# Performance work log

Hardware: AMD Instinct MI355X
Metric: run time of the kernel (lower is better)

Reference implementation:

```python
import jax, jax.numpy as jnp
import numpy as np

NUM_EXPERTS = 8
TOP_K = 2
D_MODEL = 1024
D_HID = 4096
BATCH, SEQ = 2, 2048


def setup_inputs() -> dict:
    key = jax.random.key(0)
    ks = jax.random.split(key, 5)
    s = 0.02  # param scale
    return {
        "x": jax.random.normal(ks[0], (BATCH, SEQ, D_MODEL), dtype=jnp.float32),
        "Wg": jax.random.normal(ks[1], (D_MODEL, NUM_EXPERTS), dtype=jnp.float32) * s,
        "bg": jnp.zeros((NUM_EXPERTS,), dtype=jnp.float32),
        "W0": jax.random.normal(ks[2], (NUM_EXPERTS, D_MODEL, D_HID), dtype=jnp.float32) * s,
        "b0": jnp.zeros((NUM_EXPERTS, D_HID), dtype=jnp.float32),
        "W1": jax.random.normal(ks[3], (NUM_EXPERTS, D_MODEL, D_HID), dtype=jnp.float32) * s,
        "b1": jnp.zeros((NUM_EXPERTS, D_HID), dtype=jnp.float32),
        "W2": jax.random.normal(ks[4], (NUM_EXPERTS, D_HID, D_MODEL), dtype=jnp.float32) * s,
        "b2": jnp.zeros((NUM_EXPERTS, D_MODEL), dtype=jnp.float32),
    }


def reference(x, Wg, bg, W0, b0, W1, b1, W2, b2):
    n, s, d = x.shape
    # --- routing ---
    gate_logits = x @ Wg + bg                      # [n, s, E]
    top_vals, top_idx = jax.lax.top_k(gate_logits, TOP_K)  # [n, s, K]
    w = jax.nn.softmax(top_vals, axis=-1)          # [n, s, K]
    # combine weights scattered back to dense [n, s, E]
    combine = jnp.sum(jax.nn.one_hot(top_idx, NUM_EXPERTS, dtype=x.dtype) * w[..., None], axis=-2)
    # --- dense expert compute (all experts on all tokens, masked combine) ---
    xf = x.reshape(n * s, d)                       # [T, d]
    h = jnp.einsum('td,edh->eth', xf, W0) + b0[:, None, :]   # [E, T, H]
    g = jax.nn.silu(jnp.einsum('td,edh->eth', xf, W1) + b1[:, None, :])
    y = jnp.einsum('eth,ehd->etd', h * g, W2) + b2[:, None, :]  # [E, T, d]
    out = jnp.einsum('te,etd->td', combine.reshape(n * s, NUM_EXPERTS), y)
    return out.reshape(n, s, d)
```

## Files before the change

kernel.cpp:

```cpp
#include <hip/hip_runtime.h>

#define NTOK 4096
#define DM 1024
#define DH 4096
#define NE 8

typedef __attribute__((ext_vector_type(8))) short bf16x8;
typedef __attribute__((ext_vector_type(4))) float f32x4;

__device__ __forceinline__ ushort f2bf(float f) {
  union { float f; unsigned u; } v; v.f = f;
  unsigned r = v.u + 0x7fffu + ((v.u >> 16) & 1u);
  return (ushort)(r >> 16);
}

#define GL2LDS(g, l) __builtin_amdgcn_global_load_lds( \
    (__attribute__((address_space(1))) const void*)(g), \
    (__attribute__((address_space(3))) void*)(l), 16, 0, 0)

__global__ __launch_bounds__(256) void gate_kernel(
    const float* __restrict__ x, const float* __restrict__ Wg,
    const float* __restrict__ bg, int* __restrict__ tkE,
    float* __restrict__ tkW, int* __restrict__ gcnt)
{
  const int wave = threadIdx.x >> 6;
  const int lane = threadIdx.x & 63;
  const int t = blockIdx.x * 4 + wave;

  float acc[NE];
#pragma unroll
  for (int e = 0; e < NE; e++) acc[e] = 0.f;

  for (int i = 0; i < DM / 64; i++) {
    int d = i * 64 + lane;
    float xv = x[(long)t * DM + d];
#pragma unroll
    for (int e = 0; e < NE; e++) acc[e] += xv * Wg[d * NE + e];
  }
#pragma unroll
  for (int e = 0; e < NE; e++) {
#pragma unroll
    for (int off = 32; off; off >>= 1) acc[e] += __shfl_xor(acc[e], off, 64);
    acc[e] += bg[e];
  }
  int e0 = 0; float v0 = acc[0];
#pragma unroll
  for (int e = 1; e < NE; e++) if (acc[e] > v0) { v0 = acc[e]; e0 = e; }
  int e1 = -1; float v1 = -3.4e38f;
#pragma unroll
  for (int e = 0; e < NE; e++) if (e != e0 && acc[e] > v1) { v1 = acc[e]; e1 = e; }
  float w0 = 1.f / (1.f + __expf(v1 - v0));
  float w1 = 1.f - w0;
  if (lane == 0) {
    tkE[t] = e0 | (e1 << 8);
    tkW[2 * t] = w0;
    tkW[2 * t + 1] = w1;
    atomicAdd(&gcnt[e0], 1);
    atomicAdd(&gcnt[e1], 1);
  }
}

__global__ void scan_kernel(const int* __restrict__ gcnt, int* __restrict__ offs,
                            int* __restrict__ cursor)
{
  if (threadIdx.x == 0) {
    int o = 0;
    for (int e = 0; e < NE; e++) { offs[e] = o; o += gcnt[e]; cursor[e] = 0; }
    offs[NE] = o;
  }
}

__global__ __launch_bounds__(256) void build_kernel(
    const int* __restrict__ tkE, const float* __restrict__ tkW,
    const int* __restrict__ offs, int* __restrict__ cursor,
    int* __restrict__ rmeta, float* __restrict__ rw)
{
  int t = blockIdx.x * 256 + threadIdx.x;
  int ee = tkE[t];
#pragma unroll
  for (int k = 0; k < 2; k++) {
    int e = (k == 0) ? (ee & 0xff) : (ee >> 8);
    int pos = atomicAdd(&cursor[e], 1);
    int row = offs[e] + pos;
    rmeta[row] = t * 2 + k;
    rw[row] = tkW[t * 2 + k];
  }
}

__global__ __launch_bounds__(256) void gather_kernel(
    const float* __restrict__ x, const int* __restrict__ rmeta,
    ushort* __restrict__ xg)
{
  int row = blockIdx.x;
  int t = rmeta[row] >> 1;
  const float4* src = (const float4*)(x + (long)t * DM);
  float4 v = src[threadIdx.x];
  ushort4 o = { f2bf(v.x), f2bf(v.y), f2bf(v.z), f2bf(v.w) };
  *(ushort4*)(xg + (long)row * DM + threadIdx.x * 4) = o;
}

__global__ __launch_bounds__(256) void transpose_cvt(
    const float* __restrict__ src, ushort* __restrict__ dst,
    int R, int C, long srcE, long dstE)
{
  __shared__ float tile[32][33];
  int e = blockIdx.z;
  int c0 = blockIdx.x * 32, r0 = blockIdx.y * 32;
  const float* s = src + (long)e * srcE;
  ushort* d = dst + (long)e * dstE;
  int tx = threadIdx.x;
  int ty = threadIdx.y;
#pragma unroll
  for (int i = 0; i < 32; i += 8)
    tile[ty + i][tx] = s[(long)(r0 + ty + i) * C + c0 + tx];
  __syncthreads();
#pragma unroll
  for (int i = 0; i < 32; i += 8) {
    float v = tile[tx][ty + i];
    d[(long)(c0 + ty + i) * R + r0 + tx] = f2bf(v);
  }
}

__global__ __launch_bounds__(256, 2) void gemm1_kernel(
    const ushort* __restrict__ xg, const ushort* __restrict__ Wt01,
    const float* __restrict__ b0, const float* __restrict__ b1,
    const int* __restrict__ offs, ushort* __restrict__ aout)
{
  const int e = blockIdx.z;
  const int off_e = offs[e];
  const int cnt = offs[e + 1] - off_e;
  const int mt = blockIdx.y;
  if (mt * 128 >= cnt) return;
  const int nbase = blockIdx.x * 128;

  __shared__ ushort As[128 * 32];
  __shared__ ushort Bh[128 * 32];
  __shared__ ushort Bg[128 * 32];

  const int tid = threadIdx.x;
  const int wave = tid >> 6;
  const int lane = tid & 63;
  const int wm = wave & 1;
  const int wn = wave >> 1;

  const ushort* Ap = xg + (long)(off_e + mt * 128) * DM;
  const ushort* Bhp = Wt01 + (long)e * (2 * DH) * DM + (long)nbase * DM;
  const ushort* Bgp = Bhp + (long)DH * DM;

  f32x4 acc_h[4][4], acc_g[4][4];
#pragma unroll
  for (int i = 0; i < 4; i++)
#pragma unroll
    for (int j = 0; j < 4; j++) {
      acc_h[i][j] = (f32x4){0.f, 0.f, 0.f, 0.f};
      acc_g[i][j] = (f32x4){0.f, 0.f, 0.f, 0.f};
    }

  const int soff0 = wave * 1024 + lane * 16;

  for (int k0 = 0; k0 < DM; k0 += 32) {
    __syncthreads();
#pragma unroll
    for (int s = 0; s < 2; s++) {
      int off = s * 4096 + soff0;
      int r = off >> 6;
      int ie = (off & 63) >> 1;
      long gelem = (long)r * DM + k0 + ie;
      GL2LDS(Ap + gelem, (char*)As + off);
      GL2LDS(Bhp + gelem, (char*)Bh + off);
      GL2LDS(Bgp + gelem, (char*)Bg + off);
    }
    __syncthreads();

    bf16x8 af[4], bhf[4], bgf[4];
#pragma unroll
    for (int i = 0; i < 4; i++) {
      int ro = (i * 16 + (lane & 15)) * 32 + (lane >> 4) * 8;
      af[i]  = *(const bf16x8*)&As[(wm * 64) * 32 + ro];
      bhf[i] = *(const bf16x8*)&Bh[(wn * 64) * 32 + ro];
      bgf[i] = *(const bf16x8*)&Bg[(wn * 64) * 32 + ro];
    }
#pragma unroll
    for (int i = 0; i < 4; i++)
#pragma unroll
      for (int j = 0; j < 4; j++) {
        acc_h[i][j] = __builtin_amdgcn_mfma_f32_16x16x32_bf16(af[i], bhf[j], acc_h[i][j], 0, 0, 0);
        acc_g[i][j] = __builtin_amdgcn_mfma_f32_16x16x32_bf16(af[i], bgf[j], acc_g[i][j], 0, 0, 0);
      }
  }

#pragma unroll
  for (int j = 0; j < 4; j++) {
    const int col = nbase + wn * 64 + j * 16 + (lane & 15);
    const float bb0 = b0[e * DH + col];
    const float bb1 = b1[e * DH + col];
#pragma unroll
    for (int i = 0; i < 4; i++) {
#pragma unroll
      for (int r = 0; r < 4; r++) {
        int mlocal = mt * 128 + wm * 64 + i * 16 + (lane >> 4) * 4 + r;
        if (mlocal < cnt) {
          float h = acc_h[i][j][r] + bb0;
          float g = acc_g[i][j][r] + bb1;
          float a = h * (g / (1.f + __expf(-g)));
          aout[(long)(off_e + mlocal) * DH + col] = f2bf(a);
        }
      }
    }
  }
}

__global__ __launch_bounds__(256, 2) void gemm2_kernel(
    const ushort* __restrict__ aout, const ushort* __restrict__ W2t,
    const float* __restrict__ b2, const int* __restrict__ offs,
    const int* __restrict__ rmeta, const float* __restrict__ rw,
    float* __restrict__ ybuf)
{
  const int e = blockIdx.z;
  const int off_e = offs[e];
  const int cnt = offs[e + 1] - off_e;
  const int mt = blockIdx.y;
  if (mt * 128 >= cnt) return;
  const int nbase = blockIdx.x * 128;

  __shared__ ushort As[128 * 32];
  __shared__ ushort Bs[128 * 32];

  const int tid = threadIdx.x;
  const int wave = tid >> 6;
  const int lane = tid & 63;
  const int wm = wave & 1;
  const int wn = wave >> 1;

  const ushort* Ap = aout + (long)(off_e + mt * 128) * DH;
  const ushort* Bp = W2t + (long)e * DM * DH + (long)nbase * DH;

  f32x4 acc[4][4];
#pragma unroll
  for (int i = 0; i < 4; i++)
#pragma unroll
    for (int j = 0; j < 4; j++) acc[i][j] = (f32x4){0.f, 0.f, 0.f, 0.f};

  const int soff0 = wave * 1024 + lane * 16;

  for (int k0 = 0; k0 < DH; k0 += 32) {
    __syncthreads();
#pragma unroll
    for (int s = 0; s < 2; s++) {
      int off = s * 4096 + soff0;
      int r = off >> 6;
      int ie = (off & 63) >> 1;
      long gelem = (long)r * DH + k0 + ie;
      GL2LDS(Ap + gelem, (char*)As + off);
      GL2LDS(Bp + gelem, (char*)Bs + off);
    }
    __syncthreads();

    bf16x8 af[4], bf[4];
#pragma unroll
    for (int i = 0; i < 4; i++) {
      int ro = (i * 16 + (lane & 15)) * 32 + (lane >> 4) * 8;
      af[i] = *(const bf16x8*)&As[(wm * 64) * 32 + ro];
      bf[i] = *(const bf16x8*)&Bs[(wn * 64) * 32 + ro];
    }
#pragma unroll
    for (int i = 0; i < 4; i++)
#pragma unroll
      for (int j = 0; j < 4; j++)
        acc[i][j] = __builtin_amdgcn_mfma_f32_16x16x32_bf16(af[i], bf[j], acc[i][j], 0, 0, 0);
  }

#pragma unroll
  for (int j = 0; j < 4; j++) {
    const int col = nbase + wn * 64 + j * 16 + (lane & 15);
    const float bb2 = b2[e * DM + col];
#pragma unroll
    for (int i = 0; i < 4; i++) {
#pragma unroll
      for (int r = 0; r < 4; r++) {
        int mlocal = mt * 128 + wm * 64 + i * 16 + (lane >> 4) * 4 + r;
        if (mlocal < cnt) {
          int grow = off_e + mlocal;
          float y = acc[i][j][r] + bb2;
          ybuf[(long)rmeta[grow] * DM + col] = rw[grow] * y;
        }
      }
    }
  }
}

__global__ __launch_bounds__(256) void combine_kernel(
    const float* __restrict__ ybuf, float* __restrict__ out)
{
  int idx = blockIdx.x * 256 + threadIdx.x;
  int t = idx >> 8;
  int c = (idx & 255) * 4;
  const float4 a = *(const float4*)&ybuf[(long)(2 * t) * DM + c];
  const float4 b = *(const float4*)&ybuf[(long)(2 * t + 1) * DM + c];
  float4 o = { a.x + b.x, a.y + b.y, a.z + b.z, a.w + b.w };
  *(float4*)&out[(long)t * DM + c] = o;
}

extern "C" void kernel_launch(void* const* d_in, const int* in_sizes, int n_in,
                              void* d_out, int out_size, void* d_ws, size_t ws_size,
                              hipStream_t stream) {
  const float* x  = (const float*)d_in[0];
  const float* Wg = (const float*)d_in[1];
  const float* bg = (const float*)d_in[2];
  const float* W0 = (const float*)d_in[3];
  const float* b0 = (const float*)d_in[4];
  const float* W1 = (const float*)d_in[5];
  const float* b1 = (const float*)d_in[6];
  const float* W2 = (const float*)d_in[7];
  const float* b2 = (const float*)d_in[8];
  float* out = (float*)d_out;

  char* ws = (char*)d_ws;
  ushort* Wt01 = (ushort*)(ws + 0);
  ushort* W2t  = (ushort*)(ws + 134217728);
  ushort* xg   = (ushort*)(ws + 201326592);
  ushort* aout = (ushort*)(ws + 218365952);
  float*  ybuf = (float*)(ws + 286523392);
  int*    tkE  = (int*)(ws + 320077824);
  float*  tkW  = (float*)(ws + 320094208);
  int*    rmeta= (int*)(ws + 320126976);
  float*  rw   = (float*)(ws + 320160256);
  int*    gcnt = (int*)(ws + 320193536);
  int*    offs = gcnt + 8;
  int*    cursor = gcnt + 20;

  hipMemsetAsync(gcnt, 0, 32, stream);
  gate_kernel<<<NTOK / 4, 256, 0, stream>>>(x, Wg, bg, tkE, tkW, gcnt);
  scan_kernel<<<1, 64, 0, stream>>>(gcnt, offs, cursor);
  build_kernel<<<NTOK / 256, 256, 0, stream>>>(tkE, tkW, offs, cursor, rmeta, rw);
  gather_kernel<<<2 * NTOK, 256, 0, stream>>>(x, rmeta, xg);

  transpose_cvt<<<dim3(128, 32, 8), dim3(32, 8), 0, stream>>>(
      W0, Wt01, 1024, 4096, (long)1024 * 4096, (long)8192 * 1024);
  transpose_cvt<<<dim3(128, 32, 8), dim3(32, 8), 0, stream>>>(
      W1, Wt01 + (long)4096 * 1024, 1024, 4096, (long)1024 * 4096, (long)8192 * 1024);
  transpose_cvt<<<dim3(32, 128, 8), dim3(32, 8), 0, stream>>>(
      W2, W2t, 4096, 1024, (long)4096 * 1024, (long)1024 * 4096);

  gemm1_kernel<<<dim3(32, 32, 8), 256, 0, stream>>>(xg, Wt01, b0, b1, offs, aout);
  gemm2_kernel<<<dim3(8, 32, 8), 256, 0, stream>>>(aout, W2t, b2, offs, rmeta, rw, ybuf);
  combine_kernel<<<dim3(NTOK), 256, 0, stream>>>(ybuf, out);
}
```

Measured before the change: 1.003 ms.

## Vectorize weight transpose, remap GEMM blocks across XCDs, split-K gemm2 with bias in combine

The weight transpose kernel now reads float4 rows into a wider tile and writes 16-byte bf16 vectors, replacing scalar accesses. Both GEMMs remap the flat block index so blocks sharing an expert and N-tile are spread across the eight XCDs. gemm2 splits K into two halves with separate partial output buffers, doubling the grid for occupancy. The b2 bias, weighted by routing, moves into the combine kernel, which now sums the four partials. This reuses the Wt01 workspace for ybuf after gemm1 and adds extra partial-sum traffic.

```diff
diff --git a/kernel.cpp b/kernel.cpp
--- a/kernel.cpp
+++ b/kernel.cpp
@@ -7,6 +7,7 @@
 
 typedef __attribute__((ext_vector_type(8))) short bf16x8;
 typedef __attribute__((ext_vector_type(4))) float f32x4;
+typedef __attribute__((ext_vector_type(8))) unsigned short u16x8;
 
 __device__ __forceinline__ ushort f2bf(float f) {
   union { float f; unsigned u; } v; v.f = f;
@@ -103,22 +104,33 @@
     const float* __restrict__ src, ushort* __restrict__ dst,
     int R, int C, long srcE, long dstE)
 {
-  __shared__ float tile[32][33];
-  int e = blockIdx.z;
-  int c0 = blockIdx.x * 32, r0 = blockIdx.y * 32;
+  __shared__ __align__(16) float tile[32][132];
+  const int e = blockIdx.z;
+  const int r0 = blockIdx.y * 32;
+  const int c0 = blockIdx.x * 128;
   const float* s = src + (long)e * srcE;
   ushort* d = dst + (long)e * dstE;
-  int tx = threadIdx.x;
-  int ty = threadIdx.y;
-#pragma unroll
-  for (int i = 0; i < 32; i += 8)
-    tile[ty + i][tx] = s[(long)(r0 + ty + i) * C + c0 + tx];
+  const int tid = threadIdx.x;
+  const int lr = tid >> 5;
+  const int lc4 = tid & 31;
+#pragma unroll
+  for (int p = 0; p < 4; p++) {
+    int r = p * 8 + lr;
+    float4 v = *(const float4*)&s[(long)(r0 + r) * C + c0 + lc4 * 4];
+    *(float4*)&tile[r][lc4 * 4] = v;
+  }
   __syncthreads();
-#pragma unroll
-  for (int i = 0; i < 32; i += 8) {
-    float v = tile[tx][ty + i];
-    d[(long)(c0 + ty + i) * R + r0 + tx] = f2bf(v);
-  }
+  const int oc = tid >> 1;
+  const int half = tid & 1;
+  u16x8 o0, o1;
+#pragma unroll
+  for (int j = 0; j < 8; j++) {
+    o0[j] = f2bf(tile[half * 16 + j][oc]);
+    o1[j] = f2bf(tile[half * 16 + 8 + j][oc]);
+  }
+  ushort* dp = &d[(long)(c0 + oc) * R + r0 + half * 16];
+  *(u16x8*)dp = o0;
+  *(u16x8*)(dp + 8) = o1;
 }
 
 __global__ __launch_bounds__(256, 2) void gemm1_kernel(
@@ -126,12 +138,19 @@
     const float* __restrict__ b0, const float* __restrict__ b1,
     const int* __restrict__ offs, ushort* __restrict__ aout)
 {
-  const int e = blockIdx.z;
+  const int flat = blockIdx.x + 32 * (blockIdx.y + 32 * blockIdx.z);
+  const int xcd = flat & 7;
+  const int s_ = flat >> 3;
+  const int grp = s_ >> 5;
+  const int mt = s_ & 31;
+  const int gid = grp * 8 + xcd;
+  const int e = gid >> 5;
+  const int nt = gid & 31;
+
   const int off_e = offs[e];
   const int cnt = offs[e + 1] - off_e;
-  const int mt = blockIdx.y;
   if (mt * 128 >= cnt) return;
-  const int nbase = blockIdx.x * 128;
+  const int nbase = nt * 128;
 
   __shared__ ushort As[128 * 32];
   __shared__ ushort Bh[128 * 32];
@@ -212,16 +231,24 @@
 
 __global__ __launch_bounds__(256, 2) void gemm2_kernel(
     const ushort* __restrict__ aout, const ushort* __restrict__ W2t,
-    const float* __restrict__ b2, const int* __restrict__ offs,
-    const int* __restrict__ rmeta, const float* __restrict__ rw,
-    float* __restrict__ ybuf)
-{
-  const int e = blockIdx.z;
+    const int* __restrict__ offs, const int* __restrict__ rmeta,
+    const float* __restrict__ rw, float* __restrict__ ybuf)
+{
+  const int flat = blockIdx.x + 16 * (blockIdx.y + 32 * blockIdx.z);
+  const int xcd = flat & 7;
+  const int s_ = flat >> 3;
+  const int grp = s_ >> 5;
+  const int mt = s_ & 31;
+  const int gid = grp * 8 + xcd;
+  const int e = gid >> 4;
+  const int rest = gid & 15;
+  const int nt = rest >> 1;
+  const int kc = rest & 1;
+
   const int off_e = offs[e];
   const int cnt = offs[e + 1] - off_e;
-  const int mt = blockIdx.y;
   if (mt * 128 >= cnt) return;
-  const int nbase = blockIdx.x * 128;
+  const int nbase = nt * 128;
 
   __shared__ ushort As[128 * 32];
   __shared__ ushort Bs[128 * 32];
@@ -242,8 +269,9 @@
     for (int j = 0; j < 4; j++) acc[i][j] = (f32x4){0.f, 0.f, 0.f, 0.f};
 
   const int soff0 = wave * 1024 + lane * 16;
-
-  for (int k0 = 0; k0 < DH; k0 += 32) {
+  const int kbase = kc * 2048;
+
+  for (int k0 = kbase; k0 < kbase + 2048; k0 += 32) {
     __syncthreads();
 #pragma unroll
     for (int s = 0; s < 2; s++) {
@@ -256,24 +284,23 @@
     }
     __syncthreads();
 
-    bf16x8 af[4], bf[4];
+    bf16x8 af[4], bfr[4];
 #pragma unroll
     for (int i = 0; i < 4; i++) {
       int ro = (i * 16 + (lane & 15)) * 32 + (lane >> 4) * 8;
-      af[i] = *(const bf16x8*)&As[(wm * 64) * 32 + ro];
-      bf[i] = *(const bf16x8*)&Bs[(wn * 64) * 32 + ro];
+      af[i]  = *(const bf16x8*)&As[(wm * 64) * 32 + ro];
+      bfr[i] = *(const bf16x8*)&Bs[(wn * 64) * 32 + ro];
     }
 #pragma unroll
     for (int i = 0; i < 4; i++)
 #pragma unroll
       for (int j = 0; j < 4; j++)
-        acc[i][j] = __builtin_amdgcn_mfma_f32_16x16x32_bf16(af[i], bf[j], acc[i][j], 0, 0, 0);
+        acc[i][j] = __builtin_amdgcn_mfma_f32_16x16x32_bf16(af[i], bfr[j], acc[i][j], 0, 0, 0);
   }
 
 #pragma unroll
   for (int j = 0; j < 4; j++) {
     const int col = nbase + wn * 64 + j * 16 + (lane & 15);
-    const float bb2 = b2[e * DM + col];
 #pragma unroll
     for (int i = 0; i < 4; i++) {
 #pragma unroll
@@ -281,8 +308,7 @@
         int mlocal = mt * 128 + wm * 64 + i * 16 + (lane >> 4) * 4 + r;
         if (mlocal < cnt) {
           int grow = off_e + mlocal;
-          float y = acc[i][j][r] + bb2;
-          ybuf[(long)rmeta[grow] * DM + col] = rw[grow] * y;
+          ybuf[((long)kc * 8192 + rmeta[grow]) * DM + col] = rw[grow] * acc[i][j][r];
         }
       }
     }
@@ -290,15 +316,32 @@
 }
 
 __global__ __launch_bounds__(256) void combine_kernel(
-    const float* __restrict__ ybuf, float* __restrict__ out)
-{
-  int idx = blockIdx.x * 256 + threadIdx.x;
-  int t = idx >> 8;
-  int c = (idx & 255) * 4;
-  const float4 a = *(const float4*)&ybuf[(long)(2 * t) * DM + c];
-  const float4 b = *(const float4*)&ybuf[(long)(2 * t + 1) * DM + c];
-  float4 o = { a.x + b.x, a.y + b.y, a.z + b.z, a.w + b.w };
-  *(float4*)&out[(long)t * DM + c] = o;
+    const float* __restrict__ ybuf, const int* __restrict__ tkE,
+    const float* __restrict__ tkW, const float* __restrict__ b2,
+    float* __restrict__ out)
+{
+  const int t = blockIdx.x;
+  const int c = threadIdx.x * 4;
+  const int ee = tkE[t];
+  const int e0 = ee & 0xff, e1 = ee >> 8;
+  const float w0 = tkW[2 * t], w1 = tkW[2 * t + 1];
+
+  float4 acc = {0.f, 0.f, 0.f, 0.f};
+#pragma unroll
+  for (int kc = 0; kc < 2; kc++) {
+#pragma unroll
+    for (int k = 0; k < 2; k++) {
+      const float4 v = *(const float4*)&ybuf[((long)kc * 8192 + 2 * t + k) * DM + c];
+      acc.x += v.x; acc.y += v.y; acc.z += v.z; acc.w += v.w;
+    }
+  }
+  const float4 p0 = *(const float4*)&b2[(long)e0 * DM + c];
+  const float4 p1 = *(const float4*)&b2[(long)e1 * DM + c];
+  acc.x += w0 * p0.x + w1 * p1.x;
+  acc.y += w0 * p0.y + w1 * p1.y;
+  acc.z += w0 * p0.z + w1 * p1.z;
+  acc.w += w0 * p0.w + w1 * p1.w;
+  *(float4*)&out[(long)t * DM + c] = acc;
 }
 
 extern "C" void kernel_launch(void* const* d_in, const int* in_sizes, int n_in,
@@ -317,10 +360,10 @@
 
   char* ws = (char*)d_ws;
   ushort* Wt01 = (ushort*)(ws + 0);
+  float*  ybuf = (float*)(ws + 0);
   ushort* W2t  = (ushort*)(ws + 134217728);
   ushort* xg   = (ushort*)(ws + 201326592);
   ushort* aout = (ushort*)(ws + 218365952);
-  float*  ybuf = (float*)(ws + 286523392);
   int*    tkE  = (int*)(ws + 320077824);
   float*  tkW  = (float*)(ws + 320094208);
   int*    rmeta= (int*)(ws + 320126976);
@@ -335,14 +378,14 @@
   build_kernel<<<NTOK / 256, 256, 0, stream>>>(tkE, tkW, offs, cursor, rmeta, rw);
   gather_kernel<<<2 * NTOK, 256, 0, stream>>>(x, rmeta, xg);
 
-  transpose_cvt<<<dim3(128, 32, 8), dim3(32, 8), 0, stream>>>(
+  transpose_cvt<<<dim3(32, 32, 8), 256, 0, stream>>>(
       W0, Wt01, 1024, 4096, (long)1024 * 4096, (long)8192 * 1024);
-  transpose_cvt<<<dim3(128, 32, 8), dim3(32, 8), 0, stream>>>(
+  transpose_cvt<<<dim3(32, 32, 8), 256, 0, stream>>>(
       W1, Wt01 + (long)4096 * 1024, 1024, 4096, (long)1024 * 4096, (long)8192 * 1024);
-  transpose_cvt<<<dim3(32, 128, 8), dim3(32, 8), 0, stream>>>(
+  transpose_cvt<<<dim3(8, 128, 8), 256, 0, stream>>>(
       W2, W2t, 4096, 1024, (long)4096 * 1024, (long)1024 * 4096);
 
   gemm1_kernel<<<dim3(32, 32, 8), 256, 0, stream>>>(xg, Wt01, b0, b1, offs, aout);
-  gemm2_kernel<<<dim3(8, 32, 8), 256, 0, stream>>>(aout, W2t, b2, offs, rmeta, rw, ybuf);
-  combine_kernel<<<dim3(NTOK), 256, 0, stream>>>(ybuf, out);
-}
+  gemm2_kernel<<<dim3(16, 32, 8), 256, 0, stream>>>(aout, W2t, offs, rmeta, rw, ybuf);
+  combine_kernel<<<dim3(NTOK), 256, 0, stream>>>(ybuf, tkE, tkW, b2, out);
+}
```

After: 973.6 us. 1.03x faster.
